# Performance work log

Measured on AMD Instinct MI355X. Metric: run time of the kernel, lower is better.

## Reference

```python
import jax, jax.numpy as jnp
import numpy as np

D_MODEL = 1024
NUM_HEADS = 16
DEPTH = D_MODEL // NUM_HEADS


def setup_inputs() -> dict:
    key = jax.random.key(0)
    ks = jax.random.split(key, 12)
    B, S = 2, 2048
    s = 1.0 / np.sqrt(D_MODEL)
    return {
        "q": jax.random.normal(ks[0], (B, S, D_MODEL), jnp.float32),
        "k": jax.random.normal(ks[1], (B, S, D_MODEL), jnp.float32),
        "v": jax.random.normal(ks[2], (B, S, D_MODEL), jnp.float32),
        "wq": jax.random.normal(ks[3], (D_MODEL, D_MODEL), jnp.float32) * s,
        "bq": jnp.zeros((D_MODEL,), jnp.float32),
        "wk": jax.random.normal(ks[4], (D_MODEL, D_MODEL), jnp.float32) * s,
        "bk": jnp.zeros((D_MODEL,), jnp.float32),
        "wv": jax.random.normal(ks[5], (D_MODEL, D_MODEL), jnp.float32) * s,
        "bv": jnp.zeros((D_MODEL,), jnp.float32),
        "wo": jax.random.normal(ks[6], (D_MODEL, D_MODEL), jnp.float32) * s,
        "bo": jnp.zeros((D_MODEL,), jnp.float32),
    }


def _split_heads(x):
    B, S, _ = x.shape
    return x.reshape(B, S, NUM_HEADS, DEPTH).transpose(0, 2, 1, 3)  # [B,H,S,d]


def reference(q, k, v, wq, bq, wk, bk, wv, bv, wo, bo):
    B, S, _ = q.shape
    qh = _split_heads(q @ wq + bq)
    kh = _split_heads(k @ wk + bk)
    vh = _split_heads(v @ wv + bv)
    scale = 1.0 / jnp.sqrt(jnp.asarray(DEPTH, jnp.float32))
    logits = jnp.einsum("bhqd,bhkd->bhqk", qh, kh) * scale  # [B,H,S,S]
    attn = jax.nn.softmax(logits, axis=-1)
    ctx = jnp.einsum("bhqk,bhkd->bhqd", attn, vh)
    ctx = ctx.transpose(0, 2, 1, 3).reshape(B, S, D_MODEL)
    out = ctx @ wo + bo
    return out, attn
```

## Files before the change

### kernel.cpp

```cpp
#include <hip/hip_runtime.h>
#include <math.h>

#define D_MODEL   1024
#define NUM_HEADS 16
#define DEPTH     64
#define S_LEN     2048
#define BATCH     2

typedef __attribute__((ext_vector_type(4))) float  f32x4;
typedef __attribute__((ext_vector_type(8))) __bf16 bf16x8;
typedef __attribute__((ext_vector_type(4))) __bf16 bf16x4;

__device__ __forceinline__ void split2(float x, __bf16& h, __bf16& l) {
    h = (__bf16)x;
    l = (__bf16)(x - (float)h);
}

__device__ __forceinline__ int frag_off(int r, int k) {
    return (((r >> 4) * 2 + (k >> 5)) << 10) + (((((k >> 3) & 3) << 4) + (r & 15)) << 4);
}

__device__ __forceinline__ f32x4 mm16(bf16x8 a, bf16x8 b, f32x4 c) {
    return __builtin_amdgcn_mfma_f32_16x16x32_bf16(a, b, c, 0, 0, 0);
}

__device__ __forceinline__ void store_split8(char* dh, char* dl, f32x4 x0, f32x4 x1) {
    bf16x8 vh, vl;
#pragma unroll
    for (int j = 0; j < 4; ++j) {
        __bf16 h, l;
        split2(x0[j], h, l); vh[j] = h;     vl[j] = l;
        split2(x1[j], h, l); vh[j + 4] = h; vl[j + 4] = l;
    }
    *(bf16x8*)dh = vh;
    *(bf16x8*)dl = vl;
}

__global__ __launch_bounds__(256) void wsplit(const float* __restrict__ w0,
                                              const float* __restrict__ w1,
                                              const float* __restrict__ w2,
                                              const float* __restrict__ w3,
                                              __bf16* __restrict__ hiAll,
                                              __bf16* __restrict__ loAll)
{
    const int z = blockIdx.z;
    const float* W = (z == 0) ? w0 : (z == 1) ? w1 : (z == 2) ? w2 : w3;
    __bf16* Hi = hiAll + (size_t)z * 1024 * 1024;
    __bf16* Lo = loAll + (size_t)z * 1024 * 1024;

    __shared__ float T[64][65];
    const int tid = threadIdx.x;
    const int k0 = blockIdx.x * 64, n0 = blockIdx.y * 64;
    const int rr = tid / 16, cc = (tid % 16) * 4;

#pragma unroll
    for (int p = 0; p < 4; ++p) {
        int r = p * 16 + rr;
        f32x4 v = *(const f32x4*)&W[(size_t)(k0 + r) * 1024 + n0 + cc];
        T[r][cc + 0] = v[0]; T[r][cc + 1] = v[1];
        T[r][cc + 2] = v[2]; T[r][cc + 3] = v[3];
    }
    __syncthreads();
#pragma unroll
    for (int p = 0; p < 4; ++p) {
        int nr = p * 16 + rr;
        bf16x4 vh, vl;
#pragma unroll
        for (int j = 0; j < 4; ++j) {
            __bf16 h, l;
            split2(T[cc + j][nr], h, l);
            vh[j] = h; vl[j] = l;
        }
        *(bf16x4*)&Hi[(size_t)(n0 + nr) * 1024 + k0 + cc] = vh;
        *(bf16x4*)&Lo[(size_t)(n0 + nr) * 1024 + k0 + cc] = vl;
    }
}

__global__ __launch_bounds__(512) void gemm_split(
    const float* __restrict__ A,
    const __bf16* __restrict__ BtHi, const __bf16* __restrict__ BtLo,
    const float* __restrict__ bias,
    __bf16* __restrict__ oHi, __bf16* __restrict__ oLo,
    float* __restrict__ oF, int mode)
{
    __shared__ __align__(16) char lds[65536];
    char* AH = lds;
    char* AL = lds + 16384;
    char* BH = lds + 32768;
    char* BL = lds + 49152;

    const int tid = threadIdx.x;
    const int lane = tid & 63, wid = tid >> 6;
    const int wm = wid >> 2, wn = wid & 3;
    const int bm = blockIdx.x * 128, bn = blockIdx.y * 128;

    const int r0 = tid >> 3, kc8 = (tid & 7) * 8;
    const int r1 = r0 + 64;
    const size_t a0 = (size_t)(bm + r0) * 1024 + kc8;
    const size_t a1 = (size_t)(bm + r1) * 1024 + kc8;
    const size_t b0 = (size_t)(bn + r0) * 1024 + kc8;
    const size_t b1 = (size_t)(bn + r1) * 1024 + kc8;
    const int la0 = frag_off(r0, kc8), la1 = frag_off(r1, kc8);

    const f32x4 zero = {0.f, 0.f, 0.f, 0.f};
    f32x4 acc[4][2];
#pragma unroll
    for (int i = 0; i < 4; ++i) { acc[i][0] = zero; acc[i][1] = zero; }

    f32x4 ax00 = *(const f32x4*)(A + a0);
    f32x4 ax01 = *(const f32x4*)(A + a0 + 4);
    f32x4 ax10 = *(const f32x4*)(A + a1);
    f32x4 ax11 = *(const f32x4*)(A + a1 + 4);
    bf16x8 bh0 = *(const bf16x8*)(BtHi + b0);
    bf16x8 bh1 = *(const bf16x8*)(BtHi + b1);
    bf16x8 bl0 = *(const bf16x8*)(BtLo + b0);
    bf16x8 bl1 = *(const bf16x8*)(BtLo + b1);

    for (int k0 = 0; k0 < 1024; k0 += 64) {
        __syncthreads();
        store_split8(AH + la0, AL + la0, ax00, ax01);
        store_split8(AH + la1, AL + la1, ax10, ax11);
        *(bf16x8*)(BH + la0) = bh0;
        *(bf16x8*)(BH + la1) = bh1;
        *(bf16x8*)(BL + la0) = bl0;
        *(bf16x8*)(BL + la1) = bl1;
        __syncthreads();
        if (k0 + 64 < 1024) {
            const int kn = k0 + 64;
            ax00 = *(const f32x4*)(A + a0 + kn);
            ax01 = *(const f32x4*)(A + a0 + kn + 4);
            ax10 = *(const f32x4*)(A + a1 + kn);
            ax11 = *(const f32x4*)(A + a1 + kn + 4);
            bh0 = *(const bf16x8*)(BtHi + b0 + kn);
            bh1 = *(const bf16x8*)(BtHi + b1 + kn);
            bl0 = *(const bf16x8*)(BtLo + b0 + kn);
            bl1 = *(const bf16x8*)(BtLo + b1 + kn);
        }
#pragma unroll
        for (int kf = 0; kf < 2; ++kf) {
            bf16x8 fah[4], fal[4], fbh[2], fbl[2];
#pragma unroll
            for (int mf = 0; mf < 4; ++mf) {
                const int off = (((wm * 4 + mf) * 2 + kf) << 10) + lane * 16;
                fah[mf] = *(const bf16x8*)(AH + off);
                fal[mf] = *(const bf16x8*)(AL + off);
            }
#pragma unroll
            for (int nf = 0; nf < 2; ++nf) {
                const int off = (((wn * 2 + nf) * 2 + kf) << 10) + lane * 16;
                fbh[nf] = *(const bf16x8*)(BH + off);
                fbl[nf] = *(const bf16x8*)(BL + off);
            }
#pragma unroll
            for (int mf = 0; mf < 4; ++mf)
#pragma unroll
                for (int nf = 0; nf < 2; ++nf) {
                    acc[mf][nf] = mm16(fal[mf], fbh[nf], acc[mf][nf]);
                    acc[mf][nf] = mm16(fah[mf], fbl[nf], acc[mf][nf]);
                    acc[mf][nf] = mm16(fah[mf], fbh[nf], acc[mf][nf]);
                }
        }
    }

    const int rbase = (lane >> 4) * 4;
    const int cloc = lane & 15;
#pragma unroll
    for (int mf = 0; mf < 4; ++mf) {
        const int m0g = bm + wm * 64 + mf * 16 + rbase;
#pragma unroll
        for (int nf = 0; nf < 2; ++nf) {
            const int n_g = bn + wn * 32 + nf * 16 + cloc;
            const float bv = bias[n_g];
            float v[4];
#pragma unroll
            for (int r = 0; r < 4; ++r) v[r] = acc[mf][nf][r] + bv;
            if (mode == 1) {
#pragma unroll
                for (int r = 0; r < 4; ++r) oF[(size_t)(m0g + r) * 1024 + n_g] = v[r];
            } else {
                const int bb = m0g >> 11;
                const int sloc = m0g & 2047;
                const int h = n_g >> 6, d = n_g & 63;
                if (mode == 0) {
                    const size_t i0 = ((size_t)(bb * 16 + h) * 2048 + sloc) * 64 + d;
#pragma unroll
                    for (int r = 0; r < 4; ++r) {
                        __bf16 hh, ll;
                        split2(v[r], hh, ll);
                        oHi[i0 + (size_t)r * 64] = hh;
                        oLo[i0 + (size_t)r * 64] = ll;
                    }
                } else {
                    const size_t i0 = ((size_t)(bb * 16 + h) * 64 + d) * 2048 + sloc;
                    bf16x4 vh, vl;
#pragma unroll
                    for (int r = 0; r < 4; ++r) {
                        __bf16 hh, ll;
                        split2(v[r], hh, ll);
                        vh[r] = hh; vl[r] = ll;
                    }
                    *(bf16x4*)&oHi[i0] = vh;
                    *(bf16x4*)&oLo[i0] = vl;
                }
            }
        }
    }
}

__global__ __launch_bounds__(512) void scores_mfma(
    const __bf16* __restrict__ QHi, const __bf16* __restrict__ QLo,
    const __bf16* __restrict__ KHi, const __bf16* __restrict__ KLo,
    float* __restrict__ attn)
{
    __shared__ __align__(16) char lds[65536];
    char* QH = lds;
    char* QL = lds + 16384;
    char* KH = lds + 32768;
    char* KL = lds + 49152;

    const int tid = threadIdx.x;
    const int lane = tid & 63, wid = tid >> 6;
    const int wm = wid >> 2, wn = wid & 3;
    const int m0 = blockIdx.x * 128, n0 = blockIdx.y * 128;
    const int bh = blockIdx.z;

    const __bf16* Qh_ = QHi + (size_t)bh * S_LEN * 64;
    const __bf16* Ql_ = QLo + (size_t)bh * S_LEN * 64;
    const __bf16* Kh_ = KHi + (size_t)bh * S_LEN * 64;
    const __bf16* Kl_ = KLo + (size_t)bh * S_LEN * 64;

    const int r0 = tid >> 3, kc8 = (tid & 7) * 8;
    const int r1 = r0 + 64;
    const int l0 = frag_off(r0, kc8), l1 = frag_off(r1, kc8);
    const size_t q0 = (size_t)(m0 + r0) * 64 + kc8;
    const size_t q1 = (size_t)(m0 + r1) * 64 + kc8;
    const size_t k0 = (size_t)(n0 + r0) * 64 + kc8;
    const size_t k1 = (size_t)(n0 + r1) * 64 + kc8;

    *(bf16x8*)(QH + l0) = *(const bf16x8*)(Qh_ + q0);
    *(bf16x8*)(QH + l1) = *(const bf16x8*)(Qh_ + q1);
    *(bf16x8*)(QL + l0) = *(const bf16x8*)(Ql_ + q0);
    *(bf16x8*)(QL + l1) = *(const bf16x8*)(Ql_ + q1);
    *(bf16x8*)(KH + l0) = *(const bf16x8*)(Kh_ + k0);
    *(bf16x8*)(KH + l1) = *(const bf16x8*)(Kh_ + k1);
    *(bf16x8*)(KL + l0) = *(const bf16x8*)(Kl_ + k0);
    *(bf16x8*)(KL + l1) = *(const bf16x8*)(Kl_ + k1);
    __syncthreads();

    const f32x4 zero = {0.f, 0.f, 0.f, 0.f};
    f32x4 acc[4][2];
#pragma unroll
    for (int i = 0; i < 4; ++i) { acc[i][0] = zero; acc[i][1] = zero; }

#pragma unroll
    for (int kf = 0; kf < 2; ++kf) {
        bf16x8 fah[4], fal[4], fbh[2], fbl[2];
#pragma unroll
        for (int mf = 0; mf < 4; ++mf) {
            const int off = (((wm * 4 + mf) * 2 + kf) << 10) + lane * 16;
            fah[mf] = *(const bf16x8*)(QH + off);
            fal[mf] = *(const bf16x8*)(QL + off);
        }
#pragma unroll
        for (int nf = 0; nf < 2; ++nf) {
            const int off = (((wn * 2 + nf) * 2 + kf) << 10) + lane * 16;
            fbh[nf] = *(const bf16x8*)(KH + off);
            fbl[nf] = *(const bf16x8*)(KL + off);
        }
#pragma unroll
        for (int mf = 0; mf < 4; ++mf)
#pragma unroll
            for (int nf = 0; nf < 2; ++nf) {
                acc[mf][nf] = mm16(fal[mf], fbh[nf], acc[mf][nf]);
                acc[mf][nf] = mm16(fah[mf], fbl[nf], acc[mf][nf]);
                acc[mf][nf] = mm16(fah[mf], fbh[nf], acc[mf][nf]);
            }
    }

    float* C = attn + (size_t)bh * S_LEN * S_LEN;
    const int rbase = (lane >> 4) * 4, cloc = lane & 15;
#pragma unroll
    for (int mf = 0; mf < 4; ++mf) {
        const int m0g = m0 + wm * 64 + mf * 16 + rbase;
#pragma unroll
        for (int nf = 0; nf < 2; ++nf) {
            const int n_g = n0 + wn * 32 + nf * 16 + cloc;
#pragma unroll
            for (int r = 0; r < 4; ++r)
                C[(size_t)(m0g + r) * S_LEN + n_g] = acc[mf][nf][r] * 0.125f;
        }
    }
}

__global__ __launch_bounds__(256) void softmax_kernel(float* __restrict__ attn)
{
    const size_t row = blockIdx.x;
    float* p = attn + row * (size_t)S_LEN;
    const int tid = threadIdx.x;

    float4 v0 = ((const float4*)p)[tid];
    float4 v1 = ((const float4*)p)[tid + 256];

    float m = fmaxf(fmaxf(fmaxf(v0.x, v0.y), fmaxf(v0.z, v0.w)),
                    fmaxf(fmaxf(v1.x, v1.y), fmaxf(v1.z, v1.w)));
#pragma unroll
    for (int off = 32; off > 0; off >>= 1) m = fmaxf(m, __shfl_xor(m, off));

    __shared__ float redm[4];
    __shared__ float reds[4];
    const int wave = tid >> 6, lane = tid & 63;
    if (lane == 0) redm[wave] = m;
    __syncthreads();
    m = fmaxf(fmaxf(redm[0], redm[1]), fmaxf(redm[2], redm[3]));

    v0.x = __expf(v0.x - m); v0.y = __expf(v0.y - m);
    v0.z = __expf(v0.z - m); v0.w = __expf(v0.w - m);
    v1.x = __expf(v1.x - m); v1.y = __expf(v1.y - m);
    v1.z = __expf(v1.z - m); v1.w = __expf(v1.w - m);

    float s = v0.x + v0.y + v0.z + v0.w + v1.x + v1.y + v1.z + v1.w;
#pragma unroll
    for (int off = 32; off > 0; off >>= 1) s += __shfl_xor(s, off);
    if (lane == 0) reds[wave] = s;
    __syncthreads();
    s = reds[0] + reds[1] + reds[2] + reds[3];

    const float inv = 1.0f / s;
    v0.x *= inv; v0.y *= inv; v0.z *= inv; v0.w *= inv;
    v1.x *= inv; v1.y *= inv; v1.z *= inv; v1.w *= inv;
    ((float4*)p)[tid]       = v0;
    ((float4*)p)[tid + 256] = v1;
}

__global__ __launch_bounds__(256) void ctx_mfma(
    const float* __restrict__ attn,
    const __bf16* __restrict__ VtHi, const __bf16* __restrict__ VtLo,
    float* __restrict__ ctx)
{
    __shared__ __align__(16) char lds[49152];
    char* AH = lds;
    char* AL = lds + 16384;
    char* BH = lds + 32768;
    char* BL = lds + 40960;

    const int tid = threadIdx.x;
    const int lane = tid & 63, wid = tid >> 6;
    const int wm = wid >> 1, wn = wid & 1;
    const int bm = blockIdx.x * 128;
    const int bh = blockIdx.y;
    const int bb = bh >> 4, h = bh & 15;

    const float* Ab = attn + (size_t)bh * S_LEN * S_LEN + (size_t)bm * S_LEN;
    const __bf16* Vh_ = VtHi + (size_t)bh * 64 * S_LEN;
    const __bf16* Vl_ = VtLo + (size_t)bh * 64 * S_LEN;

    const int r0 = tid >> 3, kc8 = (tid & 7) * 8;
    size_t aoff[4]; int la[4];
#pragma unroll
    for (int p = 0; p < 4; ++p) {
        aoff[p] = (size_t)(r0 + p * 32) * S_LEN + kc8;
        la[p] = frag_off(r0 + p * 32, kc8);
    }
    size_t boff[2]; int lb[2];
#pragma unroll
    for (int p = 0; p < 2; ++p) {
        boff[p] = (size_t)(r0 + p * 32) * S_LEN + kc8;
        lb[p] = frag_off(r0 + p * 32, kc8);
    }

    const f32x4 zero = {0.f, 0.f, 0.f, 0.f};
    f32x4 acc[4][2];
#pragma unroll
    for (int i = 0; i < 4; ++i) { acc[i][0] = zero; acc[i][1] = zero; }

    f32x4 ax[4][2];
    bf16x8 bxh[2], bxl[2];
#pragma unroll
    for (int p = 0; p < 4; ++p) {
        ax[p][0] = *(const f32x4*)(Ab + aoff[p]);
        ax[p][1] = *(const f32x4*)(Ab + aoff[p] + 4);
    }
#pragma unroll
    for (int p = 0; p < 2; ++p) {
        bxh[p] = *(const bf16x8*)(Vh_ + boff[p]);
        bxl[p] = *(const bf16x8*)(Vl_ + boff[p]);
    }

    for (int s0 = 0; s0 < S_LEN; s0 += 64) {
        __syncthreads();
#pragma unroll
        for (int p = 0; p < 4; ++p) store_split8(AH + la[p], AL + la[p], ax[p][0], ax[p][1]);
#pragma unroll
        for (int p = 0; p < 2; ++p) {
            *(bf16x8*)(BH + lb[p]) = bxh[p];
            *(bf16x8*)(BL + lb[p]) = bxl[p];
        }
        __syncthreads();
        if (s0 + 64 < S_LEN) {
            const int sn = s0 + 64;
#pragma unroll
            for (int p = 0; p < 4; ++p) {
                ax[p][0] = *(const f32x4*)(Ab + aoff[p] + sn);
                ax[p][1] = *(const f32x4*)(Ab + aoff[p] + sn + 4);
            }
#pragma unroll
            for (int p = 0; p < 2; ++p) {
                bxh[p] = *(const bf16x8*)(Vh_ + boff[p] + sn);
                bxl[p] = *(const bf16x8*)(Vl_ + boff[p] + sn);
            }
        }
#pragma unroll
        for (int kf = 0; kf < 2; ++kf) {
            bf16x8 fah[4], fal[4], fbh[2], fbl[2];
#pragma unroll
            for (int mf = 0; mf < 4; ++mf) {
                const int off = (((wm * 4 + mf) * 2 + kf) << 10) + lane * 16;
                fah[mf] = *(const bf16x8*)(AH + off);
                fal[mf] = *(const bf16x8*)(AL + off);
            }
#pragma unroll
            for (int nf = 0; nf < 2; ++nf) {
                const int off = (((wn * 2 + nf) * 2 + kf) << 10) + lane * 16;
                fbh[nf] = *(const bf16x8*)(BH + off);
                fbl[nf] = *(const bf16x8*)(BL + off);
            }
#pragma unroll
            for (int mf = 0; mf < 4; ++mf)
#pragma unroll
                for (int nf = 0; nf < 2; ++nf) {
                    acc[mf][nf] = mm16(fal[mf], fbh[nf], acc[mf][nf]);
                    acc[mf][nf] = mm16(fah[mf], fbl[nf], acc[mf][nf]);
                    acc[mf][nf] = mm16(fah[mf], fbh[nf], acc[mf][nf]);
                }
        }
    }

    const int rbase = (lane >> 4) * 4, cloc = lane & 15;
#pragma unroll
    for (int mf = 0; mf < 4; ++mf) {
        const int sg0 = bm + wm * 64 + mf * 16 + rbase;
#pragma unroll
        for (int nf = 0; nf < 2; ++nf) {
            const int d = wn * 32 + nf * 16 + cloc;
#pragma unroll
            for (int r = 0; r < 4; ++r)
                ctx[((size_t)bb * S_LEN + sg0 + r) * D_MODEL + h * 64 + d] = acc[mf][nf][r];
        }
    }
}

extern "C" void kernel_launch(void* const* d_in, const int* in_sizes, int n_in,
                              void* d_out, int out_size, void* d_ws, size_t ws_size,
                              hipStream_t stream)
{
    const float* q  = (const float*)d_in[0];
    const float* k  = (const float*)d_in[1];
    const float* v  = (const float*)d_in[2];
    const float* wq = (const float*)d_in[3];
    const float* bq = (const float*)d_in[4];
    const float* wk = (const float*)d_in[5];
    const float* bk = (const float*)d_in[6];
    const float* wv = (const float*)d_in[7];
    const float* bv = (const float*)d_in[8];
    const float* wo = (const float*)d_in[9];
    const float* bo = (const float*)d_in[10];

    float* out  = (float*)d_out;
    float* attn = out + (size_t)BATCH * S_LEN * D_MODEL;

    char* ws = (char*)d_ws;
    const size_t MB = 1024 * 1024;
    __bf16* WT_HI = (__bf16*)(ws);
    __bf16* WT_LO = (__bf16*)(ws + 8 * MB);
    __bf16* QHI   = (__bf16*)(ws + 16 * MB);
    __bf16* QLO   = (__bf16*)(ws + 24 * MB);
    __bf16* KHI   = (__bf16*)(ws + 32 * MB);
    __bf16* KLO   = (__bf16*)(ws + 40 * MB);
    __bf16* VTHI  = (__bf16*)(ws + 48 * MB);
    __bf16* VTLO  = (__bf16*)(ws + 56 * MB);
    float*  ctxb  = (float*)(ws + 16 * MB);
    const size_t WSTRIDE = 1024 * 1024;

    wsplit<<<dim3(16, 16, 4), dim3(256), 0, stream>>>(wq, wk, wv, wo, WT_HI, WT_LO);

    gemm_split<<<dim3(32, 8), dim3(512), 0, stream>>>(q, WT_HI + 0 * WSTRIDE, WT_LO + 0 * WSTRIDE,
                                                      bq, QHI, QLO, nullptr, 0);
    gemm_split<<<dim3(32, 8), dim3(512), 0, stream>>>(k, WT_HI + 1 * WSTRIDE, WT_LO + 1 * WSTRIDE,
                                                      bk, KHI, KLO, nullptr, 0);
    gemm_split<<<dim3(32, 8), dim3(512), 0, stream>>>(v, WT_HI + 2 * WSTRIDE, WT_LO + 2 * WSTRIDE,
                                                      bv, VTHI, VTLO, nullptr, 2);

    scores_mfma<<<dim3(16, 16, BATCH * NUM_HEADS), dim3(512), 0, stream>>>(QHI, QLO, KHI, KLO, attn);
    softmax_kernel<<<dim3(BATCH * NUM_HEADS * S_LEN), dim3(256), 0, stream>>>(attn);

    ctx_mfma<<<dim3(16, BATCH * NUM_HEADS), dim3(256), 0, stream>>>(attn, VTHI, VTLO, ctxb);

    gemm_split<<<dim3(32, 8), dim3(512), 0, stream>>>(ctxb, WT_HI + 3 * WSTRIDE, WT_LO + 3 * WSTRIDE,
                                                      bo, nullptr, nullptr, out, 1);
}
```

Measured before the change: 1.196 ms.

## Fuse scores, softmax and PV into a two-pass flash-style attention kernel

Replaces the separate scores, softmax and context kernels with one fused kernel per batch. The first pass computes running row max and sum over K tiles. The second pass recomputes QK, writes the normalized probabilities to the attention output, and accumulates P·V directly from LDS. This removes the round trip of writing the score matrix and reading it back for softmax and PV, at the cost of doing QK twice and adding several extra barriers per tile. The 1/sqrt(d) scale is folded into the Q projection epilogue. The workspace is rearranged so the output projection can run per batch after each attention launch.

```diff
diff --git a/kernel.cpp b/kernel.cpp
--- a/kernel.cpp
+++ b/kernel.cpp
@@ -16,37 +16,37 @@
     l = (__bf16)(x - (float)h);
 }
 
-__device__ __forceinline__ int frag_off(int r, int k) {
-    return (((r >> 4) * 2 + (k >> 5)) << 10) + (((((k >> 3) & 3) << 4) + (r & 15)) << 4);
+__device__ __forceinline__ int frag2(int r, int k) {
+    return (((r >> 4) * 2 + (k >> 5)) << 10) + (((k >> 3) & 3) << 8) + ((r & 15) << 4);
+}
+__device__ __forceinline__ int frag4(int r, int k) {
+    return (((r >> 4) * 4 + (k >> 5)) << 10) + (((k >> 3) & 3) << 8) + ((r & 15) << 4);
 }
 
 __device__ __forceinline__ f32x4 mm16(bf16x8 a, bf16x8 b, f32x4 c) {
     return __builtin_amdgcn_mfma_f32_16x16x32_bf16(a, b, c, 0, 0, 0);
 }
 
-__device__ __forceinline__ void store_split8(char* dh, char* dl, f32x4 x0, f32x4 x1) {
-    bf16x8 vh, vl;
+__device__ __forceinline__ void split8(f32x4 x0, f32x4 x1, bf16x8& vh, bf16x8& vl) {
 #pragma unroll
     for (int j = 0; j < 4; ++j) {
         __bf16 h, l;
         split2(x0[j], h, l); vh[j] = h;     vl[j] = l;
         split2(x1[j], h, l); vh[j + 4] = h; vl[j + 4] = l;
     }
-    *(bf16x8*)dh = vh;
-    *(bf16x8*)dl = vl;
 }
 
 __global__ __launch_bounds__(256) void wsplit(const float* __restrict__ w0,
                                               const float* __restrict__ w1,
                                               const float* __restrict__ w2,
                                               const float* __restrict__ w3,
-                                              __bf16* __restrict__ hiAll,
-                                              __bf16* __restrict__ loAll)
+                                              __bf16* __restrict__ base)
 {
     const int z = blockIdx.z;
     const float* W = (z == 0) ? w0 : (z == 1) ? w1 : (z == 2) ? w2 : w3;
-    __bf16* Hi = hiAll + (size_t)z * 1024 * 1024;
-    __bf16* Lo = loAll + (size_t)z * 1024 * 1024;
+    const size_t hi_off = (z == 3) ? 0 : (size_t)(z + 1) * 2097152;
+    __bf16* Hi = base + hi_off;
+    __bf16* Lo = Hi + 1048576;
 
     __shared__ float T[64][65];
     const int tid = threadIdx.x;
@@ -100,37 +100,34 @@
     const size_t a1 = (size_t)(bm + r1) * 1024 + kc8;
     const size_t b0 = (size_t)(bn + r0) * 1024 + kc8;
     const size_t b1 = (size_t)(bn + r1) * 1024 + kc8;
-    const int la0 = frag_off(r0, kc8), la1 = frag_off(r1, kc8);
+    const int la0 = frag2(r0, kc8), la1 = frag2(r1, kc8);
 
     const f32x4 zero = {0.f, 0.f, 0.f, 0.f};
     f32x4 acc[4][2];
 #pragma unroll
     for (int i = 0; i < 4; ++i) { acc[i][0] = zero; acc[i][1] = zero; }
 
-    f32x4 ax00 = *(const f32x4*)(A + a0);
-    f32x4 ax01 = *(const f32x4*)(A + a0 + 4);
-    f32x4 ax10 = *(const f32x4*)(A + a1);
-    f32x4 ax11 = *(const f32x4*)(A + a1 + 4);
+    f32x4 x0 = *(const f32x4*)(A + a0), x1 = *(const f32x4*)(A + a0 + 4);
+    f32x4 x2 = *(const f32x4*)(A + a1), x3 = *(const f32x4*)(A + a1 + 4);
     bf16x8 bh0 = *(const bf16x8*)(BtHi + b0);
     bf16x8 bh1 = *(const bf16x8*)(BtHi + b1);
     bf16x8 bl0 = *(const bf16x8*)(BtLo + b0);
     bf16x8 bl1 = *(const bf16x8*)(BtLo + b1);
 
     for (int k0 = 0; k0 < 1024; k0 += 64) {
-        __syncthreads();
-        store_split8(AH + la0, AL + la0, ax00, ax01);
-        store_split8(AH + la1, AL + la1, ax10, ax11);
-        *(bf16x8*)(BH + la0) = bh0;
-        *(bf16x8*)(BH + la1) = bh1;
-        *(bf16x8*)(BL + la0) = bl0;
-        *(bf16x8*)(BL + la1) = bl1;
+        bf16x8 ah0, al0, ah1, al1;
+        split8(x0, x1, ah0, al0);
+        split8(x2, x3, ah1, al1);
+        __syncthreads();
+        *(bf16x8*)(AH + la0) = ah0; *(bf16x8*)(AL + la0) = al0;
+        *(bf16x8*)(AH + la1) = ah1; *(bf16x8*)(AL + la1) = al1;
+        *(bf16x8*)(BH + la0) = bh0; *(bf16x8*)(BH + la1) = bh1;
+        *(bf16x8*)(BL + la0) = bl0; *(bf16x8*)(BL + la1) = bl1;
         __syncthreads();
         if (k0 + 64 < 1024) {
             const int kn = k0 + 64;
-            ax00 = *(const f32x4*)(A + a0 + kn);
-            ax01 = *(const f32x4*)(A + a0 + kn + 4);
-            ax10 = *(const f32x4*)(A + a1 + kn);
-            ax11 = *(const f32x4*)(A + a1 + kn + 4);
+            x0 = *(const f32x4*)(A + a0 + kn); x1 = *(const f32x4*)(A + a0 + kn + 4);
+            x2 = *(const f32x4*)(A + a1 + kn); x3 = *(const f32x4*)(A + a1 + kn + 4);
             bh0 = *(const bf16x8*)(BtHi + b0 + kn);
             bh1 = *(const bf16x8*)(BtHi + b1 + kn);
             bl0 = *(const bf16x8*)(BtLo + b0 + kn);
@@ -173,7 +170,10 @@
             const float bv = bias[n_g];
             float v[4];
 #pragma unroll
-            for (int r = 0; r < 4; ++r) v[r] = acc[mf][nf][r] + bv;
+            for (int r = 0; r < 4; ++r) {
+                v[r] = acc[mf][nf][r] + bv;
+                if (mode == 3) v[r] *= 0.125f;
+            }
             if (mode == 1) {
 #pragma unroll
                 for (int r = 0; r < 4; ++r) oF[(size_t)(m0g + r) * 1024 + n_g] = v[r];
@@ -181,7 +181,7 @@
                 const int bb = m0g >> 11;
                 const int sloc = m0g & 2047;
                 const int h = n_g >> 6, d = n_g & 63;
-                if (mode == 0) {
+                if (mode != 2) {
                     const size_t i0 = ((size_t)(bb * 16 + h) * 2048 + sloc) * 64 + d;
 #pragma unroll
                     for (int r = 0; r < 4; ++r) {
@@ -207,246 +207,282 @@
     }
 }
 
-__global__ __launch_bounds__(512) void scores_mfma(
+__global__ __launch_bounds__(512) void attn_fused(
     const __bf16* __restrict__ QHi, const __bf16* __restrict__ QLo,
     const __bf16* __restrict__ KHi, const __bf16* __restrict__ KLo,
-    float* __restrict__ attn)
+    const __bf16* __restrict__ VtHi, const __bf16* __restrict__ VtLo,
+    float* __restrict__ attn, float* __restrict__ ctxb)
 {
     __shared__ __align__(16) char lds[65536];
-    char* QH = lds;
-    char* QL = lds + 16384;
-    char* KH = lds + 32768;
-    char* KL = lds + 49152;
+    char* KV = lds;
+    char* PB = lds + 32768;
+    float* scr = (float*)PB;
 
     const int tid = threadIdx.x;
     const int lane = tid & 63, wid = tid >> 6;
     const int wm = wid >> 2, wn = wid & 3;
-    const int m0 = blockIdx.x * 128, n0 = blockIdx.y * 128;
-    const int bh = blockIdx.z;
+
+    const int id = blockIdx.x;
+    const int bh = (id & 7) + (id >> 7) * 8;
+    const int bm = ((id >> 3) & 15) * 128;
 
     const __bf16* Qh_ = QHi + (size_t)bh * S_LEN * 64;
     const __bf16* Ql_ = QLo + (size_t)bh * S_LEN * 64;
     const __bf16* Kh_ = KHi + (size_t)bh * S_LEN * 64;
     const __bf16* Kl_ = KLo + (size_t)bh * S_LEN * 64;
-
-    const int r0 = tid >> 3, kc8 = (tid & 7) * 8;
-    const int r1 = r0 + 64;
-    const int l0 = frag_off(r0, kc8), l1 = frag_off(r1, kc8);
-    const size_t q0 = (size_t)(m0 + r0) * 64 + kc8;
-    const size_t q1 = (size_t)(m0 + r1) * 64 + kc8;
-    const size_t k0 = (size_t)(n0 + r0) * 64 + kc8;
-    const size_t k1 = (size_t)(n0 + r1) * 64 + kc8;
-
-    *(bf16x8*)(QH + l0) = *(const bf16x8*)(Qh_ + q0);
-    *(bf16x8*)(QH + l1) = *(const bf16x8*)(Qh_ + q1);
-    *(bf16x8*)(QL + l0) = *(const bf16x8*)(Ql_ + q0);
-    *(bf16x8*)(QL + l1) = *(const bf16x8*)(Ql_ + q1);
-    *(bf16x8*)(KH + l0) = *(const bf16x8*)(Kh_ + k0);
-    *(bf16x8*)(KH + l1) = *(const bf16x8*)(Kh_ + k1);
-    *(bf16x8*)(KL + l0) = *(const bf16x8*)(Kl_ + k0);
-    *(bf16x8*)(KL + l1) = *(const bf16x8*)(Kl_ + k1);
-    __syncthreads();
-
-    const f32x4 zero = {0.f, 0.f, 0.f, 0.f};
-    f32x4 acc[4][2];
-#pragma unroll
-    for (int i = 0; i < 4; ++i) { acc[i][0] = zero; acc[i][1] = zero; }
-
-#pragma unroll
-    for (int kf = 0; kf < 2; ++kf) {
-        bf16x8 fah[4], fal[4], fbh[2], fbl[2];
-#pragma unroll
-        for (int mf = 0; mf < 4; ++mf) {
-            const int off = (((wm * 4 + mf) * 2 + kf) << 10) + lane * 16;
-            fah[mf] = *(const bf16x8*)(QH + off);
-            fal[mf] = *(const bf16x8*)(QL + off);
-        }
-#pragma unroll
-        for (int nf = 0; nf < 2; ++nf) {
-            const int off = (((wn * 2 + nf) * 2 + kf) << 10) + lane * 16;
-            fbh[nf] = *(const bf16x8*)(KH + off);
-            fbl[nf] = *(const bf16x8*)(KL + off);
-        }
-#pragma unroll
-        for (int mf = 0; mf < 4; ++mf)
-#pragma unroll
-            for (int nf = 0; nf < 2; ++nf) {
-                acc[mf][nf] = mm16(fal[mf], fbh[nf], acc[mf][nf]);
-                acc[mf][nf] = mm16(fah[mf], fbl[nf], acc[mf][nf]);
-                acc[mf][nf] = mm16(fah[mf], fbh[nf], acc[mf][nf]);
-            }
-    }
-
-    float* C = attn + (size_t)bh * S_LEN * S_LEN;
-    const int rbase = (lane >> 4) * 4, cloc = lane & 15;
-#pragma unroll
-    for (int mf = 0; mf < 4; ++mf) {
-        const int m0g = m0 + wm * 64 + mf * 16 + rbase;
-#pragma unroll
-        for (int nf = 0; nf < 2; ++nf) {
-            const int n_g = n0 + wn * 32 + nf * 16 + cloc;
-#pragma unroll
-            for (int r = 0; r < 4; ++r)
-                C[(size_t)(m0g + r) * S_LEN + n_g] = acc[mf][nf][r] * 0.125f;
-        }
-    }
-}
-
-__global__ __launch_bounds__(256) void softmax_kernel(float* __restrict__ attn)
-{
-    const size_t row = blockIdx.x;
-    float* p = attn + row * (size_t)S_LEN;
-    const int tid = threadIdx.x;
-
-    float4 v0 = ((const float4*)p)[tid];
-    float4 v1 = ((const float4*)p)[tid + 256];
-
-    float m = fmaxf(fmaxf(fmaxf(v0.x, v0.y), fmaxf(v0.z, v0.w)),
-                    fmaxf(fmaxf(v1.x, v1.y), fmaxf(v1.z, v1.w)));
-#pragma unroll
-    for (int off = 32; off > 0; off >>= 1) m = fmaxf(m, __shfl_xor(m, off));
-
-    __shared__ float redm[4];
-    __shared__ float reds[4];
-    const int wave = tid >> 6, lane = tid & 63;
-    if (lane == 0) redm[wave] = m;
-    __syncthreads();
-    m = fmaxf(fmaxf(redm[0], redm[1]), fmaxf(redm[2], redm[3]));
-
-    v0.x = __expf(v0.x - m); v0.y = __expf(v0.y - m);
-    v0.z = __expf(v0.z - m); v0.w = __expf(v0.w - m);
-    v1.x = __expf(v1.x - m); v1.y = __expf(v1.y - m);
-    v1.z = __expf(v1.z - m); v1.w = __expf(v1.w - m);
-
-    float s = v0.x + v0.y + v0.z + v0.w + v1.x + v1.y + v1.z + v1.w;
-#pragma unroll
-    for (int off = 32; off > 0; off >>= 1) s += __shfl_xor(s, off);
-    if (lane == 0) reds[wave] = s;
-    __syncthreads();
-    s = reds[0] + reds[1] + reds[2] + reds[3];
-
-    const float inv = 1.0f / s;
-    v0.x *= inv; v0.y *= inv; v0.z *= inv; v0.w *= inv;
-    v1.x *= inv; v1.y *= inv; v1.z *= inv; v1.w *= inv;
-    ((float4*)p)[tid]       = v0;
-    ((float4*)p)[tid + 256] = v1;
-}
-
-__global__ __launch_bounds__(256) void ctx_mfma(
-    const float* __restrict__ attn,
-    const __bf16* __restrict__ VtHi, const __bf16* __restrict__ VtLo,
-    float* __restrict__ ctx)
-{
-    __shared__ __align__(16) char lds[49152];
-    char* AH = lds;
-    char* AL = lds + 16384;
-    char* BH = lds + 32768;
-    char* BL = lds + 40960;
-
-    const int tid = threadIdx.x;
-    const int lane = tid & 63, wid = tid >> 6;
-    const int wm = wid >> 1, wn = wid & 1;
-    const int bm = blockIdx.x * 128;
-    const int bh = blockIdx.y;
-    const int bb = bh >> 4, h = bh & 15;
-
-    const float* Ab = attn + (size_t)bh * S_LEN * S_LEN + (size_t)bm * S_LEN;
     const __bf16* Vh_ = VtHi + (size_t)bh * 64 * S_LEN;
     const __bf16* Vl_ = VtLo + (size_t)bh * 64 * S_LEN;
+    float* attn_b = attn + (size_t)bh * S_LEN * S_LEN;
+
+    bf16x8 qh[4][2], ql[4][2];
+#pragma unroll
+    for (int mf = 0; mf < 4; ++mf)
+#pragma unroll
+        for (int kf = 0; kf < 2; ++kf) {
+            const int row = bm + wm * 64 + mf * 16 + (lane & 15);
+            const int k = kf * 32 + (lane >> 4) * 8;
+            qh[mf][kf] = *(const bf16x8*)(Qh_ + (size_t)row * 64 + k);
+            ql[mf][kf] = *(const bf16x8*)(Ql_ + (size_t)row * 64 + k);
+        }
 
     const int r0 = tid >> 3, kc8 = (tid & 7) * 8;
-    size_t aoff[4]; int la[4];
-#pragma unroll
-    for (int p = 0; p < 4; ++p) {
-        aoff[p] = (size_t)(r0 + p * 32) * S_LEN + kc8;
-        la[p] = frag_off(r0 + p * 32, kc8);
-    }
-    size_t boff[2]; int lb[2];
-#pragma unroll
-    for (int p = 0; p < 2; ++p) {
-        boff[p] = (size_t)(r0 + p * 32) * S_LEN + kc8;
-        lb[p] = frag_off(r0 + p * 32, kc8);
-    }
-
-    const f32x4 zero = {0.f, 0.f, 0.f, 0.f};
-    f32x4 acc[4][2];
-#pragma unroll
-    for (int i = 0; i < 4; ++i) { acc[i][0] = zero; acc[i][1] = zero; }
-
-    f32x4 ax[4][2];
-    bf16x8 bxh[2], bxl[2];
-#pragma unroll
-    for (int p = 0; p < 4; ++p) {
-        ax[p][0] = *(const f32x4*)(Ab + aoff[p]);
-        ax[p][1] = *(const f32x4*)(Ab + aoff[p] + 4);
-    }
-#pragma unroll
-    for (int p = 0; p < 2; ++p) {
-        bxh[p] = *(const bf16x8*)(Vh_ + boff[p]);
-        bxl[p] = *(const bf16x8*)(Vl_ + boff[p]);
-    }
-
-    for (int s0 = 0; s0 < S_LEN; s0 += 64) {
-        __syncthreads();
-#pragma unroll
-        for (int p = 0; p < 4; ++p) store_split8(AH + la[p], AL + la[p], ax[p][0], ax[p][1]);
-#pragma unroll
-        for (int p = 0; p < 2; ++p) {
-            *(bf16x8*)(BH + lb[p]) = bxh[p];
-            *(bf16x8*)(BL + lb[p]) = bxl[p];
-        }
-        __syncthreads();
-        if (s0 + 64 < S_LEN) {
-            const int sn = s0 + 64;
-#pragma unroll
-            for (int p = 0; p < 4; ++p) {
-                ax[p][0] = *(const f32x4*)(Ab + aoff[p] + sn);
-                ax[p][1] = *(const f32x4*)(Ab + aoff[p] + sn + 4);
-            }
-#pragma unroll
-            for (int p = 0; p < 2; ++p) {
-                bxh[p] = *(const bf16x8*)(Vh_ + boff[p] + sn);
-                bxl[p] = *(const bf16x8*)(Vl_ + boff[p] + sn);
-            }
-        }
+    const int lk0 = frag2(r0, kc8), lk1 = frag2(r0 + 64, kc8);
+    const int lv0 = frag4(r0, kc8), lv1 = frag4(r0, kc8 + 64);
+
+    auto qk_tile = [&](f32x4 (&acc)[4][2]) {
+        const f32x4 z4 = {0.f, 0.f, 0.f, 0.f};
+#pragma unroll
+        for (int i = 0; i < 4; ++i) { acc[i][0] = z4; acc[i][1] = z4; }
 #pragma unroll
         for (int kf = 0; kf < 2; ++kf) {
-            bf16x8 fah[4], fal[4], fbh[2], fbl[2];
-#pragma unroll
-            for (int mf = 0; mf < 4; ++mf) {
-                const int off = (((wm * 4 + mf) * 2 + kf) << 10) + lane * 16;
-                fah[mf] = *(const bf16x8*)(AH + off);
-                fal[mf] = *(const bf16x8*)(AL + off);
-            }
+            bf16x8 kbh[2], kbl[2];
 #pragma unroll
             for (int nf = 0; nf < 2; ++nf) {
                 const int off = (((wn * 2 + nf) * 2 + kf) << 10) + lane * 16;
-                fbh[nf] = *(const bf16x8*)(BH + off);
-                fbl[nf] = *(const bf16x8*)(BL + off);
+                kbh[nf] = *(const bf16x8*)(KV + off);
+                kbl[nf] = *(const bf16x8*)(KV + 16384 + off);
             }
 #pragma unroll
             for (int mf = 0; mf < 4; ++mf)
 #pragma unroll
                 for (int nf = 0; nf < 2; ++nf) {
-                    acc[mf][nf] = mm16(fal[mf], fbh[nf], acc[mf][nf]);
-                    acc[mf][nf] = mm16(fah[mf], fbl[nf], acc[mf][nf]);
-                    acc[mf][nf] = mm16(fah[mf], fbh[nf], acc[mf][nf]);
+                    acc[mf][nf] = mm16(ql[mf][kf], kbh[nf], acc[mf][nf]);
+                    acc[mf][nf] = mm16(qh[mf][kf], kbl[nf], acc[mf][nf]);
+                    acc[mf][nf] = mm16(qh[mf][kf], kbh[nf], acc[mf][nf]);
                 }
         }
-    }
-
-    const int rbase = (lane >> 4) * 4, cloc = lane & 15;
-#pragma unroll
-    for (int mf = 0; mf < 4; ++mf) {
-        const int sg0 = bm + wm * 64 + mf * 16 + rbase;
-#pragma unroll
-        for (int nf = 0; nf < 2; ++nf) {
-            const int d = wn * 32 + nf * 16 + cloc;
-#pragma unroll
-            for (int r = 0; r < 4; ++r)
-                ctx[((size_t)bb * S_LEN + sg0 + r) * D_MODEL + h * 64 + d] = acc[mf][nf][r];
-        }
-    }
+    };
+
+    float m_r[4][4], l_r[4][4];
+#pragma unroll
+    for (int mf = 0; mf < 4; ++mf)
+#pragma unroll
+        for (int r = 0; r < 4; ++r) { m_r[mf][r] = -INFINITY; l_r[mf][r] = 0.f; }
+
+    bf16x8 pkh0 = *(const bf16x8*)(Kh_ + (size_t)r0 * 64 + kc8);
+    bf16x8 pkh1 = *(const bf16x8*)(Kh_ + (size_t)(r0 + 64) * 64 + kc8);
+    bf16x8 pkl0 = *(const bf16x8*)(Kl_ + (size_t)r0 * 64 + kc8);
+    bf16x8 pkl1 = *(const bf16x8*)(Kl_ + (size_t)(r0 + 64) * 64 + kc8);
+
+    for (int t = 0; t < 16; ++t) {
+        __syncthreads();
+        *(bf16x8*)(KV + lk0) = pkh0; *(bf16x8*)(KV + lk1) = pkh1;
+        *(bf16x8*)(KV + 16384 + lk0) = pkl0; *(bf16x8*)(KV + 16384 + lk1) = pkl1;
+        __syncthreads();
+        if (t < 15) {
+            const size_t g = (size_t)((t + 1) * 128) * 64 + kc8;
+            pkh0 = *(const bf16x8*)(Kh_ + g + (size_t)r0 * 64);
+            pkh1 = *(const bf16x8*)(Kh_ + g + (size_t)(r0 + 64) * 64);
+            pkl0 = *(const bf16x8*)(Kl_ + g + (size_t)r0 * 64);
+            pkl1 = *(const bf16x8*)(Kl_ + g + (size_t)(r0 + 64) * 64);
+        }
+        f32x4 acc[4][2];
+        qk_tile(acc);
+#pragma unroll
+        for (int mf = 0; mf < 4; ++mf)
+#pragma unroll
+            for (int r = 0; r < 4; ++r) {
+                const float s0 = acc[mf][0][r], s1 = acc[mf][1][r];
+                const float mo = m_r[mf][r];
+                const float mn = fmaxf(mo, fmaxf(s0, s1));
+                l_r[mf][r] = l_r[mf][r] * __expf(mo - mn) + __expf(s0 - mn) + __expf(s1 - mn);
+                m_r[mf][r] = mn;
+            }
+    }
+
+#pragma unroll
+    for (int mf = 0; mf < 4; ++mf)
+#pragma unroll
+        for (int r = 0; r < 4; ++r) {
+            float m = m_r[mf][r], l = l_r[mf][r];
+#pragma unroll
+            for (int mask = 1; mask < 16; mask <<= 1) {
+                const float m2 = __shfl_xor(m, mask);
+                const float l2 = __shfl_xor(l, mask);
+                const float mm = fmaxf(m, m2);
+                l = l * __expf(m - mm) + l2 * __expf(m2 - mm);
+                m = mm;
+            }
+            m_r[mf][r] = m; l_r[mf][r] = l;
+        }
+    if ((lane & 15) == 0) {
+#pragma unroll
+        for (int mf = 0; mf < 4; ++mf)
+#pragma unroll
+            for (int r = 0; r < 4; ++r) {
+                const int row = wm * 64 + mf * 16 + (lane >> 4) * 4 + r;
+                scr[(wn * 128 + row) * 2 + 0] = m_r[mf][r];
+                scr[(wn * 128 + row) * 2 + 1] = l_r[mf][r];
+            }
+    }
+    __syncthreads();
+#pragma unroll
+    for (int mf = 0; mf < 4; ++mf)
+#pragma unroll
+        for (int r = 0; r < 4; ++r) {
+            const int row = wm * 64 + mf * 16 + (lane >> 4) * 4 + r;
+            float m = scr[row * 2 + 0], l = scr[row * 2 + 1];
+#pragma unroll
+            for (int w2 = 1; w2 < 4; ++w2) {
+                const float m2 = scr[(w2 * 128 + row) * 2 + 0];
+                const float l2 = scr[(w2 * 128 + row) * 2 + 1];
+                const float mm = fmaxf(m, m2);
+                l = l * __expf(m - mm) + l2 * __expf(m2 - mm);
+                m = mm;
+            }
+            m_r[mf][r] = m;
+            l_r[mf][r] = 1.0f / l;
+        }
+    __syncthreads();
+
+    const f32x4 zero = {0.f, 0.f, 0.f, 0.f};
+    f32x4 pv[4];
+#pragma unroll
+    for (int i = 0; i < 4; ++i) pv[i] = zero;
+
+    pkh0 = *(const bf16x8*)(Kh_ + (size_t)r0 * 64 + kc8);
+    pkh1 = *(const bf16x8*)(Kh_ + (size_t)(r0 + 64) * 64 + kc8);
+    pkl0 = *(const bf16x8*)(Kl_ + (size_t)r0 * 64 + kc8);
+    pkl1 = *(const bf16x8*)(Kl_ + (size_t)(r0 + 64) * 64 + kc8);
+
+    for (int t = 0; t < 16; ++t) {
+        __syncthreads();
+        *(bf16x8*)(KV + lk0) = pkh0; *(bf16x8*)(KV + lk1) = pkh1;
+        *(bf16x8*)(KV + 16384 + lk0) = pkl0; *(bf16x8*)(KV + 16384 + lk1) = pkl1;
+        __syncthreads();
+        bf16x8 vh0, vh1, vl0, vl1;
+        {
+            const size_t gv = (size_t)r0 * S_LEN + t * 128;
+            vh0 = *(const bf16x8*)(Vh_ + gv + kc8);
+            vh1 = *(const bf16x8*)(Vh_ + gv + kc8 + 64);
+            vl0 = *(const bf16x8*)(Vl_ + gv + kc8);
+            vl1 = *(const bf16x8*)(Vl_ + gv + kc8 + 64);
+        }
+        if (t < 15) {
+            const size_t g = (size_t)((t + 1) * 128) * 64 + kc8;
+            pkh0 = *(const bf16x8*)(Kh_ + g + (size_t)r0 * 64);
+            pkh1 = *(const bf16x8*)(Kh_ + g + (size_t)(r0 + 64) * 64);
+            pkl0 = *(const bf16x8*)(Kl_ + g + (size_t)r0 * 64);
+            pkl1 = *(const bf16x8*)(Kl_ + g + (size_t)(r0 + 64) * 64);
+        }
+        f32x4 acc[4][2];
+        qk_tile(acc);
+#pragma unroll
+        for (int mf = 0; mf < 4; ++mf) {
+            const int rg0 = bm + wm * 64 + mf * 16 + (lane >> 4) * 4;
+#pragma unroll
+            for (int nf = 0; nf < 2; ++nf) {
+                const int col = t * 128 + wn * 32 + nf * 16 + (lane & 15);
+#pragma unroll
+                for (int r = 0; r < 4; ++r) {
+                    const float p = __expf(acc[mf][nf][r] - m_r[mf][r]) * l_r[mf][r];
+                    acc[mf][nf][r] = p;
+                    attn_b[(size_t)(rg0 + r) * S_LEN + col] = p;
+                }
+            }
+        }
+        __syncthreads();
+        *(bf16x8*)(KV + lv0) = vh0; *(bf16x8*)(KV + lv1) = vh1;
+        *(bf16x8*)(KV + 16384 + lv0) = vl0; *(bf16x8*)(KV + 16384 + lv1) = vl1;
+        if (wn < 2) {
+#pragma unroll
+            for (int mf = 0; mf < 4; ++mf)
+#pragma unroll
+                for (int nf = 0; nf < 2; ++nf) {
+                    const int k = (wn & 1) * 32 + nf * 16 + (lane & 15);
+#pragma unroll
+                    for (int r = 0; r < 4; ++r) {
+                        const int rl = wm * 64 + mf * 16 + (lane >> 4) * 4 + r;
+                        const int off = (((rl >> 4) * 2 + (k >> 5)) << 10) +
+                                        (((k >> 3) & 3) << 8) + ((rl & 15) << 4) + ((k & 7) << 1);
+                        __bf16 h, l;
+                        split2(acc[mf][nf][r], h, l);
+                        *(__bf16*)(PB + off) = h;
+                        *(__bf16*)(PB + 16384 + off) = l;
+                    }
+                }
+        }
+        __syncthreads();
+#pragma unroll
+        for (int kf = 0; kf < 2; ++kf) {
+            const int offv = ((wn * 4 + 0 + kf) << 10) + lane * 16;
+            const bf16x8 vhf = *(const bf16x8*)(KV + offv);
+            const bf16x8 vlf = *(const bf16x8*)(KV + 16384 + offv);
+#pragma unroll
+            for (int mf = 0; mf < 4; ++mf) {
+                const int offp = (((wm * 4 + mf) * 2 + kf) << 10) + lane * 16;
+                const bf16x8 ph = *(const bf16x8*)(PB + offp);
+                const bf16x8 pl = *(const bf16x8*)(PB + 16384 + offp);
+                pv[mf] = mm16(pl, vhf, pv[mf]);
+                pv[mf] = mm16(ph, vlf, pv[mf]);
+                pv[mf] = mm16(ph, vhf, pv[mf]);
+            }
+        }
+        __syncthreads();
+        if (wn >= 2) {
+#pragma unroll
+            for (int mf = 0; mf < 4; ++mf)
+#pragma unroll
+                for (int nf = 0; nf < 2; ++nf) {
+                    const int k = (wn & 1) * 32 + nf * 16 + (lane & 15);
+#pragma unroll
+                    for (int r = 0; r < 4; ++r) {
+                        const int rl = wm * 64 + mf * 16 + (lane >> 4) * 4 + r;
+                        const int off = (((rl >> 4) * 2 + (k >> 5)) << 10) +
+                                        (((k >> 3) & 3) << 8) + ((rl & 15) << 4) + ((k & 7) << 1);
+                        __bf16 h, l;
+                        split2(acc[mf][nf][r], h, l);
+                        *(__bf16*)(PB + off) = h;
+                        *(__bf16*)(PB + 16384 + off) = l;
+                    }
+                }
+        }
+        __syncthreads();
+#pragma unroll
+        for (int kf = 0; kf < 2; ++kf) {
+            const int offv = ((wn * 4 + 2 + kf) << 10) + lane * 16;
+            const bf16x8 vhf = *(const bf16x8*)(KV + offv);
+            const bf16x8 vlf = *(const bf16x8*)(KV + 16384 + offv);
+#pragma unroll
+            for (int mf = 0; mf < 4; ++mf) {
+                const int offp = (((wm * 4 + mf) * 2 + kf) << 10) + lane * 16;
+                const bf16x8 ph = *(const bf16x8*)(PB + offp);
+                const bf16x8 pl = *(const bf16x8*)(PB + 16384 + offp);
+                pv[mf] = mm16(pl, vhf, pv[mf]);
+                pv[mf] = mm16(ph, vlf, pv[mf]);
+                pv[mf] = mm16(ph, vhf, pv[mf]);
+            }
+        }
+    }
+
+#pragma unroll
+    for (int mf = 0; mf < 4; ++mf)
+#pragma unroll
+        for (int r = 0; r < 4; ++r) {
+            const int sg = bm + wm * 64 + mf * 16 + (lane >> 4) * 4 + r;
+            const int d = wn * 16 + (lane & 15);
+            ctxb[(size_t)sg * 1024 + bh * 64 + d] = pv[mf][r];
+        }
 }
 
 extern "C" void kernel_launch(void* const* d_in, const int* in_sizes, int n_in,
@@ -470,31 +506,35 @@
 
     char* ws = (char*)d_ws;
     const size_t MB = 1024 * 1024;
-    __bf16* WT_HI = (__bf16*)(ws);
-    __bf16* WT_LO = (__bf16*)(ws + 8 * MB);
-    __bf16* QHI   = (__bf16*)(ws + 16 * MB);
-    __bf16* QLO   = (__bf16*)(ws + 24 * MB);
-    __bf16* KHI   = (__bf16*)(ws + 32 * MB);
-    __bf16* KLO   = (__bf16*)(ws + 40 * MB);
-    __bf16* VTHI  = (__bf16*)(ws + 48 * MB);
-    __bf16* VTLO  = (__bf16*)(ws + 56 * MB);
-    float*  ctxb  = (float*)(ws + 16 * MB);
-    const size_t WSTRIDE = 1024 * 1024;
-
-    wsplit<<<dim3(16, 16, 4), dim3(256), 0, stream>>>(wq, wk, wv, wo, WT_HI, WT_LO);
-
-    gemm_split<<<dim3(32, 8), dim3(512), 0, stream>>>(q, WT_HI + 0 * WSTRIDE, WT_LO + 0 * WSTRIDE,
-                                                      bq, QHI, QLO, nullptr, 0);
-    gemm_split<<<dim3(32, 8), dim3(512), 0, stream>>>(k, WT_HI + 1 * WSTRIDE, WT_LO + 1 * WSTRIDE,
-                                                      bk, KHI, KLO, nullptr, 0);
-    gemm_split<<<dim3(32, 8), dim3(512), 0, stream>>>(v, WT_HI + 2 * WSTRIDE, WT_LO + 2 * WSTRIDE,
-                                                      bv, VTHI, VTLO, nullptr, 2);
-
-    scores_mfma<<<dim3(16, 16, BATCH * NUM_HEADS), dim3(512), 0, stream>>>(QHI, QLO, KHI, KLO, attn);
-    softmax_kernel<<<dim3(BATCH * NUM_HEADS * S_LEN), dim3(256), 0, stream>>>(attn);
-
-    ctx_mfma<<<dim3(16, BATCH * NUM_HEADS), dim3(256), 0, stream>>>(attn, VTHI, VTLO, ctxb);
-
-    gemm_split<<<dim3(32, 8), dim3(512), 0, stream>>>(ctxb, WT_HI + 3 * WSTRIDE, WT_LO + 3 * WSTRIDE,
-                                                      bo, nullptr, nullptr, out, 1);
-}
+    __bf16* WB   = (__bf16*)ws;
+    __bf16* QHI  = (__bf16*)(ws + 16 * MB);
+    __bf16* QLO  = (__bf16*)(ws + 24 * MB);
+    __bf16* KHI  = (__bf16*)(ws + 32 * MB);
+    __bf16* KLO  = (__bf16*)(ws + 40 * MB);
+    __bf16* VTHI = (__bf16*)(ws + 48 * MB);
+    __bf16* VTLO = (__bf16*)(ws + 56 * MB);
+    float*  ctxb = (float*)(ws + 4 * MB);
+
+    const size_t W1M = 1048576;
+    __bf16* WOT_HI = WB;                  __bf16* WOT_LO = WB + W1M;
+    __bf16* WQT_HI = WB + 2 * W1M;        __bf16* WQT_LO = WB + 3 * W1M;
+    __bf16* WKT_HI = WB + 4 * W1M;        __bf16* WKT_LO = WB + 5 * W1M;
+    __bf16* WVT_HI = WB + 6 * W1M;        __bf16* WVT_LO = WB + 7 * W1M;
+
+    wsplit<<<dim3(16, 16, 4), dim3(256), 0, stream>>>(wq, wk, wv, wo, WB);
+
+    gemm_split<<<dim3(32, 8), dim3(512), 0, stream>>>(q, WQT_HI, WQT_LO, bq, QHI, QLO, nullptr, 3);
+    gemm_split<<<dim3(32, 8), dim3(512), 0, stream>>>(k, WKT_HI, WKT_LO, bk, KHI, KLO, nullptr, 0);
+    gemm_split<<<dim3(32, 8), dim3(512), 0, stream>>>(v, WVT_HI, WVT_LO, bv, VTHI, VTLO, nullptr, 2);
+
+    const size_t HOFF = (size_t)NUM_HEADS * S_LEN * DEPTH;
+    for (int b = 0; b < BATCH; ++b) {
+        attn_fused<<<dim3(256), dim3(512), 0, stream>>>(
+            QHI + b * HOFF, QLO + b * HOFF, KHI + b * HOFF, KLO + b * HOFF,
+            VTHI + b * HOFF, VTLO + b * HOFF,
+            attn + (size_t)b * NUM_HEADS * S_LEN * S_LEN, ctxb);
+        gemm_split<<<dim3(16, 8), dim3(512), 0, stream>>>(
+            ctxb, WOT_HI, WOT_LO, bo, nullptr, nullptr,
+            out + (size_t)b * S_LEN * D_MODEL, 1);
+    }
+}
```

Result: faster. 1.086 ms (-9.2%).
